# Performance work log

Hardware: AMD Instinct MI355X
Metric: run time of the kernel (lower is better)

The kernel has to match this reference:

```python
import jax, jax.numpy as jnp
import numpy as np

V, T, D, H, L, F, B = 50257, 1024, 1024, 16, 10, 4096, 2
HD = D // H  # head_dim = 64
EPS = 1e-5


def sinusoidal_pos(seq_len, d_model):
    pos = np.arange(seq_len)[:, None].astype(np.float32)
    i = np.arange(d_model // 2).astype(np.float32)
    inv = 1.0 / (10000.0 ** (2.0 * i / d_model))
    ang = pos * inv[None, :]
    pe = np.zeros((seq_len, d_model), dtype=np.float32)
    pe[:, 0::2] = np.sin(ang)
    pe[:, 1::2] = np.cos(ang)
    return jnp.asarray(pe)


def setup_inputs() -> dict:
    key = jax.random.key(0)
    ks = jax.random.split(key, 16)
    s = 0.02
    return {
        "x": jax.random.randint(ks[0], (B, T), 0, V),
        "emb": jax.random.normal(ks[1], (V, D), jnp.float32) * s,
        "pos": sinusoidal_pos(T, D),
        "Wq": jax.random.normal(ks[2], (L, D, D), jnp.float32) * s,
        "bq": jnp.zeros((L, D), jnp.float32),
        "Wk": jax.random.normal(ks[3], (L, D, D), jnp.float32) * s,
        "bk": jnp.zeros((L, D), jnp.float32),
        "Wv": jax.random.normal(ks[4], (L, D, D), jnp.float32) * s,
        "bv": jnp.zeros((L, D), jnp.float32),
        "ln_g": jnp.ones((L, D), jnp.float32),
        "ln_b": jnp.zeros((L, D), jnp.float32),
        "W1": jax.random.normal(ks[5], (L, D, F), jnp.float32) * s,
        "b1": jnp.zeros((L, F), jnp.float32),
        "W2": jax.random.normal(ks[6], (L, F, D), jnp.float32) * s,
        "b2": jnp.zeros((L, D), jnp.float32),
        "lnf_g": jnp.ones((D,), jnp.float32),
        "lnf_b": jnp.zeros((D,), jnp.float32),
        "Wout": jax.random.normal(ks[7], (D, V), jnp.float32) * s,
        "bout": jnp.zeros((V,), jnp.float32),
    }


def layer_norm(h, g, b):
    mu = jnp.mean(h, axis=-1, keepdims=True)
    var = jnp.mean(jnp.square(h - mu), axis=-1, keepdims=True)
    return (h - mu) * jax.lax.rsqrt(var + EPS) * g + b


def reference(x, emb, pos, Wq, bq, Wk, bk, Wv, bv, ln_g, ln_b, W1, b1, W2, b2, lnf_g, lnf_b, Wout, bout):
    t = x.shape[1]
    h = emb[x] + pos[None, :t]  # [B,T,D]
    causal = jnp.tril(jnp.ones((t, t), bool))  # True = keep
    scale = 1.0 / jnp.sqrt(jnp.float32(HD))

    def body(h, p):
        wq, bq_, wk, bk_, wv, bv_, g, bln, w1, b1_, w2, b2_ = p
        q = (h @ wq + bq_).reshape(B, t, H, HD)
        k = (h @ wk + bk_).reshape(B, t, H, HD)
        v = (h @ wv + bv_).reshape(B, t, H, HD)
        score = jnp.einsum('bqhd,bkhd->bhqk', q, k) * scale
        score = jnp.where(causal, score, -jnp.inf)
        attn = jax.nn.softmax(score, axis=-1)
        o = jnp.einsum('bhqk,bkhd->bqhd', attn, v).reshape(B, t, D)
        h = layer_norm(h + o, g, bln)
        m = jax.nn.gelu(h @ w1 + b1_, approximate=False) @ w2 + b2_
        h = layer_norm(h + m, g, bln)  # same LayerNorm params reused, as in source
        return h, None

    h, _ = jax.lax.scan(body, h, (Wq, bq, Wk, bk, Wv, bv, ln_g, ln_b, W1, b1, W2, b2))
    h = layer_norm(h, lnf_g, lnf_b)
    return h @ Wout + bout  # [B,T,V]
```

## Files before the change

kernel.cpp:

```cpp
#include <hip/hip_runtime.h>
#include <cstdint>
#include <cstddef>

#define Vv 50257
#define Va 50304
#define Tt 1024
#define Dd 1024
#define Hh 16
#define Ll 10
#define Ff 4096
#define Bb 2
#define Mm (Bb*Tt)

typedef float f32x4 __attribute__((ext_vector_type(4)));
typedef __bf16 bf16x8 __attribute__((ext_vector_type(8)));
typedef unsigned short u16x8 __attribute__((ext_vector_type(8)));
typedef unsigned short u16x4 __attribute__((ext_vector_type(4)));

static __device__ __forceinline__ unsigned short f2bf(float f) {
  unsigned int u = __builtin_bit_cast(unsigned int, f);
  unsigned int r = (u + 0x7FFFu + ((u >> 16) & 1u)) >> 16;
  return (unsigned short)r;
}

static __device__ __forceinline__ f32x4 mfma16x16x32(u16x8 a, u16x8 b, f32x4 c) {
  return __builtin_amdgcn_mfma_f32_16x16x32_bf16(
      __builtin_bit_cast(bf16x8, a), __builtin_bit_cast(bf16x8, b), c, 0, 0, 0);
}

static __device__ __forceinline__ void async_cp16(const void* g, void* l) {
  __builtin_amdgcn_global_load_lds(
      (const __attribute__((address_space(1))) unsigned int*)g,
      (__attribute__((address_space(3))) unsigned int*)l, 16, 0, 0);
}

__global__ __launch_bounds__(256) void embed_kernel(
    const int* __restrict__ x, const float* __restrict__ emb,
    const float* __restrict__ pos, float* __restrict__ h,
    unsigned short* __restrict__ hb) {
  int bt = blockIdx.x;
  int t = bt & (Tt - 1);
  int tok = x[bt];
  int i = threadIdx.x * 4;
  f32x4 e = *(const f32x4*)(emb + (size_t)tok * Dd + i);
  f32x4 p = *(const f32x4*)(pos + (size_t)t * Dd + i);
  f32x4 r = e + p;
  *(f32x4*)(h + (size_t)bt * Dd + i) = r;
  u16x4 rb = { f2bf(r[0]), f2bf(r[1]), f2bf(r[2]), f2bf(r[3]) };
  *(u16x4*)(hb + (size_t)bt * Dd + i) = rb;
}

__global__ __launch_bounds__(256) void add_ln_kernel(
    const float* __restrict__ hin, const float* __restrict__ r,
    const float* __restrict__ g, const float* __restrict__ bb,
    float* __restrict__ hout, unsigned short* __restrict__ hbout) {
  int row = blockIdx.x;
  int tid = threadIdx.x;
  size_t off = (size_t)row * Dd + tid * 4;
  f32x4 xv = *(const f32x4*)(hin + off);
  if (r) xv += *(const f32x4*)(r + off);
  float s  = xv[0] + xv[1] + xv[2] + xv[3];
  float ss = xv[0]*xv[0] + xv[1]*xv[1] + xv[2]*xv[2] + xv[3]*xv[3];
  #pragma unroll
  for (int o = 1; o < 64; o <<= 1) {
    s  += __shfl_xor(s, o);
    ss += __shfl_xor(ss, o);
  }
  __shared__ float red[8];
  int wave = tid >> 6, lane = tid & 63;
  if (lane == 0) { red[wave] = s; red[4 + wave] = ss; }
  __syncthreads();
  s  = red[0] + red[1] + red[2] + red[3];
  ss = red[4] + red[5] + red[6] + red[7];
  float mu = s * (1.0f / Dd);
  float var = ss * (1.0f / Dd) - mu * mu;
  float rstd = rsqrtf(var + 1e-5f);
  f32x4 gv = *(const f32x4*)(g + tid * 4);
  f32x4 bv = *(const f32x4*)(bb + tid * 4);
  f32x4 y;
  #pragma unroll
  for (int j = 0; j < 4; ++j) y[j] = (xv[j] - mu) * rstd * gv[j] + bv[j];
  *(f32x4*)(hout + off) = y;
  u16x4 yb = { f2bf(y[0]), f2bf(y[1]), f2bf(y[2]), f2bf(y[3]) };
  *(u16x4*)(hbout + off) = yb;
}

__global__ __launch_bounds__(256) void bias_gather_kernel(
    const float* __restrict__ bq, const float* __restrict__ bk,
    const float* __restrict__ bv, float* __restrict__ cb) {
  int l = blockIdx.x;
  int i = threadIdx.x * 4;
  f32x4 q = *(const f32x4*)(bq + (size_t)l * Dd + i);
  f32x4 k = *(const f32x4*)(bk + (size_t)l * Dd + i);
  f32x4 v = *(const f32x4*)(bv + (size_t)l * Dd + i);
  *(f32x4*)(cb + (size_t)l * 3072 + i) = q;
  *(f32x4*)(cb + (size_t)l * 3072 + 1024 + i) = k;
  *(f32x4*)(cb + (size_t)l * 3072 + 2048 + i) = v;
}

__global__ __launch_bounds__(256) void tconv_kernel(
    const float* __restrict__ W, unsigned short* __restrict__ Wt,
    int K, int N, int Nvalid, size_t sW, size_t sWt) {
  const float* Wl = W + (size_t)blockIdx.z * sW;
  unsigned short* Wtl = Wt + (size_t)blockIdx.z * sWt;
  __shared__ unsigned short t[64][72];
  int n0 = blockIdx.x * 64, k0 = blockIdx.y * 64;
  int tx = threadIdx.x & 15, ty = threadIdx.x >> 4;
  #pragma unroll
  for (int i = 0; i < 4; ++i) {
    int kr = ty + i * 16;
    int nc = tx * 4;
    int gn = n0 + nc;
    f32x4 v = {0.f, 0.f, 0.f, 0.f};
    if (gn + 3 < Nvalid) {
      v = *(const f32x4*)(Wl + (size_t)(k0 + kr) * N + gn);
    } else {
      #pragma unroll
      for (int j = 0; j < 4; ++j)
        if (gn + j < Nvalid) v[j] = Wl[(size_t)(k0 + kr) * N + gn + j];
    }
    t[nc + 0][kr] = f2bf(v[0]); t[nc + 1][kr] = f2bf(v[1]);
    t[nc + 2][kr] = f2bf(v[2]); t[nc + 3][kr] = f2bf(v[3]);
  }
  __syncthreads();
  #pragma unroll
  for (int i = 0; i < 4; ++i) {
    int nr = ty + i * 16;
    u16x4 o = *(const u16x4*)&t[nr][tx * 4];
    *(u16x4*)(Wtl + (size_t)(n0 + nr) * K + k0 + tx * 4) = o;
  }
}

template <int BM, int EPI, bool SWZ>
__global__ __launch_bounds__(256) void gemm_bt(
    const unsigned short* __restrict__ A, const unsigned short* __restrict__ Bt,
    const float* __restrict__ bias, void* __restrict__ Cout,
    int Ncols, int K) {
  constexpr int NJ = (BM == 128) ? 4 : 2;
  __shared__ __align__(16) unsigned short Al[2][BM * 32];
  __shared__ __align__(16) unsigned short Bl[2][128 * 32];
  int bx = blockIdx.x, by = blockIdx.y;
  if constexpr (SWZ) {
    unsigned gx = gridDim.x;
    unsigned total = gx * gridDim.y;
    unsigned flat = by * gx + bx;
    unsigned per = total >> 3;
    unsigned work = (flat & 7u) * per + (flat >> 3);
    bx = work % gx; by = work / gx;
  }
  const int bm = bx * BM;
  const int bn = by * 128;
  const int tid = threadIdx.x, lane = tid & 63, wave = tid >> 6;
  const int wm = (BM == 128) ? (wave >> 1) * 64 : 0;
  const int wn = (BM == 128) ? (wave & 1) * 64 : wave * 32;
  const int rowi = lane >> 2;
  const int koff = (lane & 3) * 8;

  auto stage = [&](int buf, int k0) {
    #pragma unroll
    for (int i = 0; i < BM / 64; ++i) {
      int ch = wave + i * 4;
      async_cp16(A + (size_t)(bm + ch * 16 + rowi) * K + k0 + koff, &Al[buf][ch * 512]);
    }
    #pragma unroll
    for (int i = 0; i < 2; ++i) {
      int ch = wave + i * 4;
      async_cp16(Bt + (size_t)(bn + ch * 16 + rowi) * K + k0 + koff, &Bl[buf][ch * 512]);
    }
  };

  f32x4 acc[4][NJ];
  #pragma unroll
  for (int i = 0; i < 4; ++i)
    #pragma unroll
    for (int j = 0; j < NJ; ++j) acc[i][j] = {0.f, 0.f, 0.f, 0.f};

  stage(0, 0);
  __syncthreads();
  int cur = 0;
  for (int k0 = 0; k0 < K; k0 += 32) {
    if (k0 + 32 < K) stage(cur ^ 1, k0 + 32);
    u16x8 af[4], bfr[NJ];
    #pragma unroll
    for (int i = 0; i < 4; ++i)
      af[i] = *(const u16x8*)&Al[cur][(wm + i * 16 + (lane & 15)) * 32 + (lane >> 4) * 8];
    #pragma unroll
    for (int j = 0; j < NJ; ++j)
      bfr[j] = *(const u16x8*)&Bl[cur][(wn + j * 16 + (lane & 15)) * 32 + (lane >> 4) * 8];
    #pragma unroll
    for (int i = 0; i < 4; ++i)
      #pragma unroll
      for (int j = 0; j < NJ; ++j)
        acc[i][j] = mfma16x16x32(af[i], bfr[j], acc[i][j]);
    __syncthreads();
    cur ^= 1;
  }

  float bvv[NJ];
  #pragma unroll
  for (int j = 0; j < NJ; ++j) {
    int col = bn + wn + j * 16 + (lane & 15);
    bvv[j] = (col < Ncols) ? bias[col] : 0.0f;
  }
  #pragma unroll
  for (int i = 0; i < 4; ++i) {
    #pragma unroll
    for (int rr = 0; rr < 4; ++rr) {
      int row = bm + wm + i * 16 + (lane >> 4) * 4 + rr;
      #pragma unroll
      for (int j = 0; j < NJ; ++j) {
        int col = bn + wn + j * 16 + (lane & 15);
        if (col < Ncols) {
          float val = acc[i][j][rr] + bvv[j];
          if constexpr (EPI == 0) {
            ((float*)Cout)[(size_t)row * Ncols + col] = val;
          } else if constexpr (EPI == 1) {
            ((unsigned short*)Cout)[(size_t)row * Ncols + col] = f2bf(val);
          } else {
            float gv = 0.5f * val * (1.0f + erff(val * 0.70710678f));
            ((unsigned short*)Cout)[(size_t)row * Ncols + col] = f2bf(gv);
          }
        }
      }
    }
  }
}

template <int EPI>
__global__ __launch_bounds__(256) void gemm_f32b(
    const unsigned short* __restrict__ A, const float* __restrict__ Bw,
    const float* __restrict__ bias, void* __restrict__ Cout, int N, int K) {
  __shared__ __align__(16) unsigned short Al[128][40];
  __shared__ __align__(16) unsigned short Btl[128][40];
  const int bn = blockIdx.x * 128;
  const int bm = blockIdx.y * 128;
  const int tid = threadIdx.x;
  const int lane = tid & 63;
  const int wave = tid >> 6;
  const int wm = (wave >> 1) * 64;
  const int wn = (wave & 1) * 64;
  const bool nfast = ((N & 3) == 0);

  f32x4 acc[4][4];
  #pragma unroll
  for (int i = 0; i < 4; ++i)
    #pragma unroll
    for (int j = 0; j < 4; ++j) acc[i][j] = {0.f, 0.f, 0.f, 0.f};

  for (int k0 = 0; k0 < K; k0 += 32) {
    __syncthreads();
    #pragma unroll
    for (int i = 0; i < 2; ++i) {
      int c = tid + i * 256;
      int row = c >> 2, ko = (c & 3) * 8;
      u16x8 v = *(const u16x8*)(A + (size_t)(bm + row) * K + k0 + ko);
      *(u16x8*)&Al[row][ko] = v;
    }
    if (nfast) {
      #pragma unroll
      for (int i = 0; i < 4; ++i) {
        int c = tid + i * 256;
        int kr = c >> 5;
        int no = (c & 31) * 4;
        f32x4 v4 = *(const f32x4*)(Bw + (size_t)(k0 + kr) * N + bn + no);
        Btl[no + 0][kr] = f2bf(v4[0]); Btl[no + 1][kr] = f2bf(v4[1]);
        Btl[no + 2][kr] = f2bf(v4[2]); Btl[no + 3][kr] = f2bf(v4[3]);
      }
    } else {
      #pragma unroll
      for (int i = 0; i < 4; ++i) {
        int c = tid + i * 256;
        int kr = c >> 5;
        int nb = c & 31;
        #pragma unroll
        for (int j = 0; j < 4; ++j) {
          int col = nb + j * 32;
          float v = (bn + col < N) ? Bw[(size_t)(k0 + kr) * N + bn + col] : 0.0f;
          Btl[col][kr] = f2bf(v);
        }
      }
    }
    __syncthreads();
    u16x8 af[4], bfr[4];
    #pragma unroll
    for (int i = 0; i < 4; ++i)
      af[i] = *(const u16x8*)&Al[wm + i * 16 + (lane & 15)][(lane >> 4) * 8];
    #pragma unroll
    for (int j = 0; j < 4; ++j)
      bfr[j] = *(const u16x8*)&Btl[wn + j * 16 + (lane & 15)][(lane >> 4) * 8];
    #pragma unroll
    for (int i = 0; i < 4; ++i)
      #pragma unroll
      for (int j = 0; j < 4; ++j)
        acc[i][j] = mfma16x16x32(af[i], bfr[j], acc[i][j]);
  }
  #pragma unroll
  for (int j = 0; j < 4; ++j) {
    int col = bn + wn + j * 16 + (lane & 15);
    bool cok = (col < N);
    float bv = cok ? bias[col] : 0.0f;
    #pragma unroll
    for (int i = 0; i < 4; ++i) {
      #pragma unroll
      for (int rr = 0; rr < 4; ++rr) {
        int row = bm + wm + i * 16 + (lane >> 4) * 4 + rr;
        float val = acc[i][j][rr] + bv;
        if (cok) {
          if constexpr (EPI == 0) ((float*)Cout)[(size_t)row * N + col] = val;
          else if constexpr (EPI == 1) ((unsigned short*)Cout)[(size_t)row * N + col] = f2bf(val);
          else {
            float gv = 0.5f * val * (1.0f + erff(val * 0.70710678f));
            ((unsigned short*)Cout)[(size_t)row * N + col] = f2bf(gv);
          }
        }
      }
    }
  }
}

__global__ __launch_bounds__(256) void attn_kernel(
    const unsigned short* __restrict__ q, const unsigned short* __restrict__ k,
    const unsigned short* __restrict__ v, float* __restrict__ o, int ld) {
  const int ys = blockIdx.y;
  const int qt = (ys < 8) ? ys : 23 - ys;
  const int bh = blockIdx.x;
  const int b = bh >> 4, h = bh & 15;
  const size_t base = (size_t)b * Tt * ld + (size_t)h * 64;
  const int tid = threadIdx.x, lane = tid & 63, wave = tid >> 6;
  const int q0 = qt * 64 + wave * 16;

  __shared__ __align__(16) unsigned short Kl[2][64][72];
  __shared__ __align__(16) unsigned short Vt[2][64][72];
  __shared__ __align__(16) unsigned short Pl[4][16][72];

  const float SC = 0.18033688011112042f;

  u16x8 qa[2];
  {
    const unsigned short* qp = q + base + (size_t)(q0 + (lane & 15)) * ld + (lane >> 4) * 8;
    qa[0] = *(const u16x8*)qp;
    qa[1] = *(const u16x8*)(qp + 32);
  }

  auto stageKV = [&](int buf, int kt) {
    #pragma unroll
    for (int i = 0; i < 2; ++i) {
      int c = tid + i * 256;
      int rr = c >> 3, dof = (c & 7) * 8;
      *(u16x8*)&Kl[buf][rr][dof] =
          *(const u16x8*)(k + base + (size_t)(kt * 64 + rr) * ld + dof);
      u16x8 vv = *(const u16x8*)(v + base + (size_t)(kt * 64 + rr) * ld + dof);
      #pragma unroll
      for (int j = 0; j < 8; ++j) {
        int d = dof + j;
        Vt[buf][d][(rr + (d & 56)) & 63] = vv[j];
      }
    }
  };

  f32x4 Oacc[4];
  #pragma unroll
  for (int df = 0; df < 4; ++df) Oacc[df] = {0.f, 0.f, 0.f, 0.f};
  float m_run[4], l_run[4];
  #pragma unroll
  for (int rr = 0; rr < 4; ++rr) { m_run[rr] = -__builtin_inff(); l_run[rr] = 0.f; }

  stageKV(0, 0);
  __syncthreads();
  int cur = 0;
  for (int kt = 0; kt <= qt; ++kt) {
    if (kt < qt) stageKV(cur ^ 1, kt + 1);

    f32x4 S[4];
    #pragma unroll
    for (int nf = 0; nf < 4; ++nf) {
      S[nf] = {0.f, 0.f, 0.f, 0.f};
      #pragma unroll
      for (int s = 0; s < 2; ++s) {
        u16x8 kb = *(const u16x8*)&Kl[cur][nf * 16 + (lane & 15)][s * 32 + (lane >> 4) * 8];
        S[nf] = mfma16x16x32(qa[s], kb, S[nf]);
      }
    }
    const int kbase = kt * 64;
    float mx[4];
    #pragma unroll
    for (int rr = 0; rr < 4; ++rr) mx[rr] = -__builtin_inff();
    #pragma unroll
    for (int nf = 0; nf < 4; ++nf) {
      int kcol = kbase + nf * 16 + (lane & 15);
      #pragma unroll
      for (int rr = 0; rr < 4; ++rr) {
        int qrow = q0 + (lane >> 4) * 4 + rr;
        float sv = S[nf][rr] * SC;
        if (kcol > qrow) sv = -__builtin_inff();
        S[nf][rr] = sv;
        mx[rr] = fmaxf(mx[rr], sv);
      }
    }
    #pragma unroll
    for (int rr = 0; rr < 4; ++rr) {
      #pragma unroll
      for (int off = 1; off < 16; off <<= 1)
        mx[rr] = fmaxf(mx[rr], __shfl_xor(mx[rr], off));
    }
    float psum[4];
    #pragma unroll
    for (int rr = 0; rr < 4; ++rr) {
      float mnew = fmaxf(m_run[rr], mx[rr]);
      float sc = exp2f(m_run[rr] - mnew);
      l_run[rr] *= sc;
      #pragma unroll
      for (int df = 0; df < 4; ++df) Oacc[df][rr] *= sc;
      m_run[rr] = mnew;
      psum[rr] = 0.f;
    }
    #pragma unroll
    for (int nf = 0; nf < 4; ++nf) {
      #pragma unroll
      for (int rr = 0; rr < 4; ++rr) {
        float pv = exp2f(S[nf][rr] - m_run[rr]);
        S[nf][rr] = pv;
        psum[rr] += pv;
      }
    }
    #pragma unroll
    for (int rr = 0; rr < 4; ++rr) {
      #pragma unroll
      for (int off = 1; off < 16; off <<= 1) psum[rr] += __shfl_xor(psum[rr], off);
      l_run[rr] += psum[rr];
    }
    #pragma unroll
    for (int nf = 0; nf < 4; ++nf)
      #pragma unroll
      for (int rr = 0; rr < 4; ++rr)
        Pl[wave][(lane >> 4) * 4 + rr][nf * 16 + (lane & 15)] = f2bf(S[nf][rr]);
    __builtin_amdgcn_sched_barrier(0);
    asm volatile("s_waitcnt lgkmcnt(0)" ::: "memory");
    __builtin_amdgcn_sched_barrier(0);
    #pragma unroll
    for (int s = 0; s < 2; ++s) {
      u16x8 pa = *(const u16x8*)&Pl[wave][lane & 15][s * 32 + (lane >> 4) * 8];
      #pragma unroll
      for (int df = 0; df < 4; ++df) {
        int d = df * 16 + (lane & 15);
        int cs = (s * 32 + (lane >> 4) * 8 + (d & 56)) & 63;
        u16x8 vb = *(const u16x8*)&Vt[cur][d][cs];
        Oacc[df] = mfma16x16x32(pa, vb, Oacc[df]);
      }
    }
    __syncthreads();
    cur ^= 1;
  }

  #pragma unroll
  for (int df = 0; df < 4; ++df) {
    int d = df * 16 + (lane & 15);
    #pragma unroll
    for (int rr = 0; rr < 4; ++rr) {
      int qrow = q0 + (lane >> 4) * 4 + rr;
      o[((size_t)b * Tt + qrow) * Dd + h * 64 + d] = Oacc[df][rr] / l_run[rr];
    }
  }
}

extern "C" void kernel_launch(void* const* d_in, const int* in_sizes, int n_in,
                              void* d_out, int out_size, void* d_ws, size_t ws_size,
                              hipStream_t stream) {
  const int*   x     = (const int*)d_in[0];
  const float* emb   = (const float*)d_in[1];
  const float* pos   = (const float*)d_in[2];
  const float* Wq    = (const float*)d_in[3];
  const float* bq    = (const float*)d_in[4];
  const float* Wk    = (const float*)d_in[5];
  const float* bk    = (const float*)d_in[6];
  const float* Wv    = (const float*)d_in[7];
  const float* bv    = (const float*)d_in[8];
  const float* ln_g  = (const float*)d_in[9];
  const float* ln_b  = (const float*)d_in[10];
  const float* W1    = (const float*)d_in[11];
  const float* b1    = (const float*)d_in[12];
  const float* W2    = (const float*)d_in[13];
  const float* b2    = (const float*)d_in[14];
  const float* lnf_g = (const float*)d_in[15];
  const float* lnf_b = (const float*)d_in[16];
  const float* Wout  = (const float*)d_in[17];
  const float* bout  = (const float*)d_in[18];
  float* out = (float*)d_out;

  char* p = (char*)d_ws;
  auto alloc = [&](size_t bytes) {
    char* r = p; p += (bytes + 255) & ~(size_t)255; return r;
  };
  float* h           = (float*)alloc((size_t)Mm * Dd * 4);
  unsigned short* hb = (unsigned short*)alloc((size_t)Mm * Dd * 2);
  unsigned short* qkv = (unsigned short*)alloc((size_t)Mm * 3072 * 2);
  float* of          = (float*)alloc((size_t)Mm * Dd * 4);
  unsigned short* a1 = (unsigned short*)alloc((size_t)Mm * Ff * 2);
  float* cb          = (float*)alloc((size_t)Ll * 3072 * 4);
  size_t base_used = (size_t)(p - (char*)d_ws);

  const size_t SZ_WQKVT = (size_t)Ll * 3072 * Dd * 2;
  const size_t SZ_W1T   = (size_t)Ll * Ff * Dd * 2;
  const size_t SZ_W2T   = (size_t)Ll * Dd * Ff * 2;
  const size_t SZ_WOUTT = (size_t)Va * Dd * 2;
  const size_t need_big = base_used + SZ_WQKVT + SZ_W1T + SZ_W2T + SZ_WOUTT + 4096;
  const size_t need_rot = base_used + SZ_WOUTT + 4096;

  embed_kernel<<<Mm, 256, 0, stream>>>(x, emb, pos, h, hb);

  if (ws_size >= need_rot) {
    bias_gather_kernel<<<Ll, 256, 0, stream>>>(bq, bk, bv, cb);
    const bool big = (ws_size >= need_big);
    unsigned short *wqkvt, *w1t, *w2t, *woutt;
    if (big) {
      wqkvt = (unsigned short*)alloc(SZ_WQKVT);
      w1t   = (unsigned short*)alloc(SZ_W1T);
      w2t   = (unsigned short*)alloc(SZ_W2T);
      woutt = (unsigned short*)alloc(SZ_WOUTT);
      tconv_kernel<<<dim3(16, 16, Ll), 256, 0, stream>>>(
          Wq, wqkvt,           Dd, Dd, Dd, (size_t)Dd*Dd, (size_t)3072*Dd);
      tconv_kernel<<<dim3(16, 16, Ll), 256, 0, stream>>>(
          Wk, wqkvt + 1024*Dd, Dd, Dd, Dd, (size_t)Dd*Dd, (size_t)3072*Dd);
      tconv_kernel<<<dim3(16, 16, Ll), 256, 0, stream>>>(
          Wv, wqkvt + 2048*Dd, Dd, Dd, Dd, (size_t)Dd*Dd, (size_t)3072*Dd);
      tconv_kernel<<<dim3(Ff/64, Dd/64, Ll), 256, 0, stream>>>(
          W1, w1t, Dd, Ff, Ff, (size_t)Dd*Ff, (size_t)Ff*Dd);
      tconv_kernel<<<dim3(Dd/64, Ff/64, Ll), 256, 0, stream>>>(
          W2, w2t, Ff, Dd, Dd, (size_t)Ff*Dd, (size_t)Dd*Ff);
      tconv_kernel<<<dim3(Va/64, Dd/64, 1), 256, 0, stream>>>(
          Wout, woutt, Dd, Vv, Vv, 0, 0);
    } else {
      unsigned short* wbuf = (unsigned short*)alloc(SZ_WOUTT);
      wqkvt = w1t = w2t = woutt = wbuf;
    }

    for (int l = 0; l < Ll; ++l) {
      unsigned short* wq_l = big ? (wqkvt + (size_t)l * 3072 * Dd) : wqkvt;
      if (!big) {
        tconv_kernel<<<dim3(16, 16, 1), 256, 0, stream>>>(Wq + (size_t)l * Dd * Dd, wq_l,           Dd, Dd, Dd, 0, 0);
        tconv_kernel<<<dim3(16, 16, 1), 256, 0, stream>>>(Wk + (size_t)l * Dd * Dd, wq_l + 1024*Dd, Dd, Dd, Dd, 0, 0);
        tconv_kernel<<<dim3(16, 16, 1), 256, 0, stream>>>(Wv + (size_t)l * Dd * Dd, wq_l + 2048*Dd, Dd, Dd, Dd, 0, 0);
      }
      gemm_bt<128, 1, false><<<dim3(Mm/128, 3072/128), 256, 0, stream>>>(
          hb, wq_l, cb + (size_t)l * 3072, qkv, 3072, Dd);
      attn_kernel<<<dim3(Bb*Hh, Tt/64), 256, 0, stream>>>(qkv, qkv + 1024, qkv + 2048, of, 3072);
      add_ln_kernel<<<Mm, 256, 0, stream>>>(h, of, ln_g + (size_t)l * Dd,
                                            ln_b + (size_t)l * Dd, h, hb);
      unsigned short* w1_l = big ? (w1t + (size_t)l * Ff * Dd) : w1t;
      if (!big)
        tconv_kernel<<<dim3(Ff/64, Dd/64, 1), 256, 0, stream>>>(W1 + (size_t)l * Dd * Ff, w1_l, Dd, Ff, Ff, 0, 0);
      gemm_bt<128, 2, false><<<dim3(Mm/128, Ff/128), 256, 0, stream>>>(
          hb, w1_l, b1 + (size_t)l * Ff, a1, Ff, Dd);
      unsigned short* w2_l = big ? (w2t + (size_t)l * Dd * Ff) : w2t;
      if (!big)
        tconv_kernel<<<dim3(Dd/64, Ff/64, 1), 256, 0, stream>>>(W2 + (size_t)l * Ff * Dd, w2_l, Ff, Dd, Dd, 0, 0);
      gemm_bt<64, 0, false><<<dim3(Mm/64, Dd/128), 256, 0, stream>>>(
          a1, w2_l, b2 + (size_t)l * Dd, of, Dd, Ff);
      add_ln_kernel<<<Mm, 256, 0, stream>>>(h, of, ln_g + (size_t)l * Dd,
                                            ln_b + (size_t)l * Dd, h, hb);
    }

    add_ln_kernel<<<Mm, 256, 0, stream>>>(h, nullptr, lnf_g, lnf_b, h, hb);
    if (!big)
      tconv_kernel<<<dim3(Va/64, Dd/64, 1), 256, 0, stream>>>(Wout, woutt, Dd, Vv, Vv, 0, 0);
    gemm_bt<128, 0, true><<<dim3(Mm/128, Va/128), 256, 0, stream>>>(
        hb, woutt, bout, out, Vv, Dd);
  } else {
    unsigned short* qb = qkv;
    unsigned short* kb = qkv + (size_t)Mm * Dd;
    unsigned short* vb = qkv + (size_t)2 * Mm * Dd;
    for (int l = 0; l < Ll; ++l) {
      const size_t wo = (size_t)l * Dd * Dd;
      gemm_f32b<1><<<dim3(Dd/128, Mm/128), 256, 0, stream>>>(hb, Wq + wo, bq + (size_t)l*Dd, qb, Dd, Dd);
      gemm_f32b<1><<<dim3(Dd/128, Mm/128), 256, 0, stream>>>(hb, Wk + wo, bk + (size_t)l*Dd, kb, Dd, Dd);
      gemm_f32b<1><<<dim3(Dd/128, Mm/128), 256, 0, stream>>>(hb, Wv + wo, bv + (size_t)l*Dd, vb, Dd, Dd);
      attn_kernel<<<dim3(Bb*Hh, Tt/64), 256, 0, stream>>>(qb, kb, vb, of, Dd);
      add_ln_kernel<<<Mm, 256, 0, stream>>>(h, of, ln_g + (size_t)l*Dd, ln_b + (size_t)l*Dd, h, hb);
      gemm_f32b<2><<<dim3(Ff/128, Mm/128), 256, 0, stream>>>(hb, W1 + (size_t)l*Dd*Ff, b1 + (size_t)l*Ff, a1, Ff, Dd);
      gemm_f32b<0><<<dim3(Dd/128, Mm/128), 256, 0, stream>>>(a1, W2 + (size_t)l*Ff*Dd, b2 + (size_t)l*Dd, of, Dd, Ff);
      add_ln_kernel<<<Mm, 256, 0, stream>>>(h, of, ln_g + (size_t)l*Dd, ln_b + (size_t)l*Dd, h, hb);
    }
    add_ln_kernel<<<Mm, 256, 0, stream>>>(h, nullptr, lnf_g, lnf_b, h, hb);
    gemm_f32b<0><<<dim3((Vv + 127)/128, Mm/128), 256, 0, stream>>>(hb, Wout, bout, out, Vv, Dd);
  }
}
```

Baseline: 2.609 ms.

## Use 128-wide KV tiles with async K copy and drop double buffering in attention

The attention kernel now processes 128 keys per iteration instead of 64, halving loop trips and the per-tile softmax reductions. K is loaded with async 16-byte copies into an XOR-swizzled unpadded LDS buffer, while V is still transposed through registers. The double buffer is replaced by a single buffer with two barriers per iteration, so load latency is no longer overlapped with compute. Larger tiles mean more wasted masked work on diagonal tiles, and the nkt formula assumes the 64-row query tile maps into 128-key tiles correctly.

```diff
diff --git a/kernel.cpp b/kernel.cpp
--- a/kernel.cpp
+++ b/kernel.cpp
@@ -329,9 +329,9 @@
   const int tid = threadIdx.x, lane = tid & 63, wave = tid >> 6;
   const int q0 = qt * 64 + wave * 16;
 
-  __shared__ __align__(16) unsigned short Kl[2][64][72];
-  __shared__ __align__(16) unsigned short Vt[2][64][72];
-  __shared__ __align__(16) unsigned short Pl[4][16][72];
+  __shared__ __align__(16) unsigned short Kl[128][64];
+  __shared__ __align__(16) unsigned short Vt[64][136];
+  __shared__ __align__(16) unsigned short Pl[4][16][136];
 
   const float SC = 0.18033688011112042f;
 
@@ -342,52 +342,59 @@
     qa[1] = *(const u16x8*)(qp + 32);
   }
 
-  auto stageKV = [&](int buf, int kt) {
-    #pragma unroll
-    for (int i = 0; i < 2; ++i) {
+  f32x4 Oacc[4];
+  #pragma unroll
+  for (int df = 0; df < 4; ++df) Oacc[df] = {0.f, 0.f, 0.f, 0.f};
+  float m_run[4], l_run[4];
+  #pragma unroll
+  for (int rr = 0; rr < 4; ++rr) { m_run[rr] = -__builtin_inff(); l_run[rr] = 0.f; }
+
+  const int r8 = lane >> 3;
+  const int kslot = (lane & 7) ^ r8;
+
+  const int nkt = (qt >> 1) + 1;
+  for (int kt = 0; kt < nkt; ++kt) {
+    __syncthreads();
+    {
+      const unsigned short* src = k + base + (size_t)kt * 128 * ld;
+      #pragma unroll
+      for (int i = 0; i < 4; ++i) {
+        int ch = wave * 4 + i;
+        async_cp16(src + (size_t)(ch * 8 + r8) * ld + kslot * 8, &Kl[ch * 8][0]);
+      }
+    }
+    #pragma unroll
+    for (int i = 0; i < 4; ++i) {
       int c = tid + i * 256;
-      int rr = c >> 3, dof = (c & 7) * 8;
-      *(u16x8*)&Kl[buf][rr][dof] =
-          *(const u16x8*)(k + base + (size_t)(kt * 64 + rr) * ld + dof);
-      u16x8 vv = *(const u16x8*)(v + base + (size_t)(kt * 64 + rr) * ld + dof);
+      int kr = c >> 3, dof = (c & 7) * 8;
+      u16x8 vv = *(const u16x8*)(v + base + (size_t)(kt * 128 + kr) * ld + dof);
       #pragma unroll
       for (int j = 0; j < 8; ++j) {
         int d = dof + j;
-        Vt[buf][d][(rr + (d & 56)) & 63] = vv[j];
-      }
-    }
-  };
-
-  f32x4 Oacc[4];
-  #pragma unroll
-  for (int df = 0; df < 4; ++df) Oacc[df] = {0.f, 0.f, 0.f, 0.f};
-  float m_run[4], l_run[4];
-  #pragma unroll
-  for (int rr = 0; rr < 4; ++rr) { m_run[rr] = -__builtin_inff(); l_run[rr] = 0.f; }
-
-  stageKV(0, 0);
-  __syncthreads();
-  int cur = 0;
-  for (int kt = 0; kt <= qt; ++kt) {
-    if (kt < qt) stageKV(cur ^ 1, kt + 1);
-
-    f32x4 S[4];
-    #pragma unroll
-    for (int nf = 0; nf < 4; ++nf) {
+        Vt[d][(kr + ((d & 56) << 1)) & 127] = vv[j];
+      }
+    }
+    __syncthreads();
+
+    f32x4 S[8];
+    #pragma unroll
+    for (int nf = 0; nf < 8; ++nf) {
       S[nf] = {0.f, 0.f, 0.f, 0.f};
+      int kcol = nf * 16 + (lane & 15);
       #pragma unroll
       for (int s = 0; s < 2; ++s) {
-        u16x8 kb = *(const u16x8*)&Kl[cur][nf * 16 + (lane & 15)][s * 32 + (lane >> 4) * 8];
+        int slot = (s * 4 + (lane >> 4)) ^ (kcol & 7);
+        u16x8 kb = *(const u16x8*)&Kl[kcol][slot * 8];
         S[nf] = mfma16x16x32(qa[s], kb, S[nf]);
       }
     }
-    const int kbase = kt * 64;
+    const int kb0 = kt * 128;
     float mx[4];
     #pragma unroll
     for (int rr = 0; rr < 4; ++rr) mx[rr] = -__builtin_inff();
     #pragma unroll
-    for (int nf = 0; nf < 4; ++nf) {
-      int kcol = kbase + nf * 16 + (lane & 15);
+    for (int nf = 0; nf < 8; ++nf) {
+      int kcol = kb0 + nf * 16 + (lane & 15);
       #pragma unroll
       for (int rr = 0; rr < 4; ++rr) {
         int qrow = q0 + (lane >> 4) * 4 + rr;
@@ -415,7 +422,7 @@
       psum[rr] = 0.f;
     }
     #pragma unroll
-    for (int nf = 0; nf < 4; ++nf) {
+    for (int nf = 0; nf < 8; ++nf) {
       #pragma unroll
       for (int rr = 0; rr < 4; ++rr) {
         float pv = exp2f(S[nf][rr] - m_run[rr]);
@@ -430,7 +437,7 @@
       l_run[rr] += psum[rr];
     }
     #pragma unroll
-    for (int nf = 0; nf < 4; ++nf)
+    for (int nf = 0; nf < 8; ++nf)
       #pragma unroll
       for (int rr = 0; rr < 4; ++rr)
         Pl[wave][(lane >> 4) * 4 + rr][nf * 16 + (lane & 15)] = f2bf(S[nf][rr]);
@@ -438,18 +445,16 @@
     asm volatile("s_waitcnt lgkmcnt(0)" ::: "memory");
     __builtin_amdgcn_sched_barrier(0);
     #pragma unroll
-    for (int s = 0; s < 2; ++s) {
+    for (int s = 0; s < 4; ++s) {
       u16x8 pa = *(const u16x8*)&Pl[wave][lane & 15][s * 32 + (lane >> 4) * 8];
       #pragma unroll
       for (int df = 0; df < 4; ++df) {
         int d = df * 16 + (lane & 15);
-        int cs = (s * 32 + (lane >> 4) * 8 + (d & 56)) & 63;
-        u16x8 vb = *(const u16x8*)&Vt[cur][d][cs];
+        int cs = (s * 32 + (lane >> 4) * 8 + ((d & 56) << 1)) & 127;
+        u16x8 vb = *(const u16x8*)&Vt[d][cs];
         Oacc[df] = mfma16x16x32(pa, vb, Oacc[df]);
       }
     }
-    __syncthreads();
-    cur ^= 1;
   }
 
   #pragma unroll
```

Result: faster. 2.553 ms (-2.2%).
